# Optimization experiments

Measured on AMD Instinct MI355X. Metric: run time of the kernel, lower is better.

The kernel has to match this reference:

```python
import math
import jax, jax.numpy as jnp
import numpy as np

B, N = 1, 512
C_S, C_Z, H, C, P_Q, P_V = 384, 128, 12, 16, 4, 8
CAT = C_Z * H + C * H + 3 * H * P_V + 1  # 2017


def _apply(t_r, t_t, x):
    # t_r: (b,n,3,3), t_t: (b,n,3), x: (b,3,h,p,n) -> global frame coords
    xg = jnp.einsum('bnij,bjhpn->bihpn', t_r, x)
    return xg + jnp.swapaxes(t_t, 1, 2)[:, :, None, None, :]


def setup_inputs() -> dict:
    key = jax.random.key(0)
    ks = jax.random.split(key, 14)
    f = lambda k, shp: jax.random.normal(k, shp, dtype=jnp.float32)
    return {
        's': f(ks[0], (B, C_S, N)),
        'z': f(ks[1], (B, C_Z, N, N)),
        't_r': f(ks[2], (B, N, 3, 3)),
        't_t': f(ks[3], (B, N, 3)),
        'Wq': f(ks[4], (C * H, C_S)) * 0.02,
        'Wk': f(ks[5], (C * H, C_S)) * 0.02,
        'Wv': f(ks[6], (C * H, C_S)) * 0.02,
        'Wqp': f(ks[7], (3 * H * P_Q, C_S)) * 0.02,
        'Wkp': f(ks[8], (3 * H * P_Q, C_S)) * 0.02,
        'Wvp': f(ks[9], (3 * H * P_V, C_S)) * 0.02,
        'Wb': f(ks[10], (H, C_Z)) * 0.02,
        'gamma': f(ks[11], (H, 1, 1)) * 0.5,
        'Ws': f(ks[12], (C_S, CAT)) * 0.02,
        'bs': jnp.zeros((C_S,), dtype=jnp.float32),
    }


def reference(s, z, t_r, t_t, Wq, Wk, Wv, Wqp, Wkp, Wvp, Wb, gamma, Ws, bs):
    b, _, n = s.shape
    w_c = math.sqrt(2.0 / (9.0 * P_Q))
    w_l = math.sqrt(1.0 / 3.0)

    proj = lambda W: jnp.einsum('oc,bcn->bon', W, s)
    # torch rearrange 'b (c h) i -> b c h i' == reshape(b, c, h, n)
    q = proj(Wq).reshape(b, C, H, n)
    k = proj(Wk).reshape(b, C, H, n)
    v = proj(Wv).reshape(b, C, H, n)
    qp = proj(Wqp).reshape(b, 3, H, P_Q, n)
    kp = proj(Wkp).reshape(b, 3, H, P_Q, n)
    vp = proj(Wvp).reshape(b, 3, H, P_V, n)

    qg = _apply(t_r, t_t, qp)  # (b,3,h,p,n)
    kg = _apply(t_r, t_t, kp)
    diff = qg[..., :, None] - kg[..., None, :]          # (b,3,h,p,n,n)
    dist2 = jnp.sum(diff * diff, axis=(1, 3))           # sum coords + points -> (b,h,n,n)
    tmp = jax.nn.softplus(gamma)[None] * (w_c / 2.0) * dist2

    b_bias = jnp.einsum('hc,bcij->bhij', Wb, z)
    qk = jnp.einsum('bchi,bchj->bhij', q, k) / math.sqrt(C)
    a = jax.nn.softmax(w_l * (qk + b_bias - tmp), axis=-1)  # (b,h,n,n)

    o1 = jnp.einsum('bhij,bcij->bchi', a, z).reshape(b, C_Z * H, n)
    o2 = jnp.einsum('bhij,bchj->bchi', a, v).reshape(b, C * H, n)

    vg = _apply(t_r, t_t, vp)                           # (b,3,h,pv,n)
    o3g = jnp.einsum('bhij,bchpj->bchpi', a, vg)        # (b,3,h,pv,n)
    t_r_inv = jnp.swapaxes(t_r, -1, -2)
    t_t_inv = jnp.einsum('bnij,bnj->bni', -t_r_inv, t_t)
    o3 = _apply(t_r_inv, t_t_inv, o3g).reshape(b, 3 * H * P_V, n)
    o3_norm = jnp.linalg.norm(o3, axis=1, keepdims=True)  # (b,1,n)

    cat = jnp.concatenate([o1, o2, o3, o3_norm], axis=1)  # (b, CAT, n)
    return jnp.einsum('oc,bcn->bon', Ws, cat) + bs[None, :, None]
```

## Files before the change

kernel.cpp:

```cpp
#include <hip/hip_runtime.h>
#include <math.h>

#define N 512
#define H 12
#define CC 16
#define CZ 128
#define CS 384
#define PQ 4
#define PV 8
#define CATR 2017

__global__ __launch_bounds__(256) void k_proj(
    const float* __restrict__ s,
    const float* __restrict__ Wq, const float* __restrict__ Wk, const float* __restrict__ Wv,
    const float* __restrict__ Wqp, const float* __restrict__ Wkp, const float* __restrict__ Wvp,
    float* __restrict__ proj)
{
    __shared__ float Wt[16][33];
    __shared__ float St[32][128];
    int t = threadIdx.x;
    int o0 = blockIdx.x * 16;
    int n0 = blockIdx.y * 128;
    const float* Wsrc; int orow;
    if (o0 < 192)      { Wsrc = Wq;  orow = o0; }
    else if (o0 < 384) { Wsrc = Wk;  orow = o0-192; }
    else if (o0 < 576) { Wsrc = Wv;  orow = o0-384; }
    else if (o0 < 720) { Wsrc = Wqp; orow = o0-576; }
    else if (o0 < 864) { Wsrc = Wkp; orow = o0-720; }
    else               { Wsrc = Wvp; orow = o0-864; }

    int og = t >> 6, nl = t & 63;
    float acc[4][2] = {};
    for (int c0 = 0; c0 < CS; c0 += 32) {
        __syncthreads();
        for (int k = 0; k < 2; k++) {
            int idx = t + k*256;
            int oo = idx >> 5, ccol = idx & 31;
            Wt[oo][ccol] = Wsrc[(orow+oo)*CS + c0 + ccol];
        }
        for (int k = 0; k < 4; k++) {
            int idx = t + k*256;
            int ccr = idx >> 5, nn4 = idx & 31;
            float4 v = *(const float4*)&s[(c0+ccr)*N + n0 + nn4*4];
            *(float4*)&St[ccr][nn4*4] = v;
        }
        __syncthreads();
        for (int kk = 0; kk < 32; kk++) {
            float sv0 = St[kk][nl], sv1 = St[kk][nl+64];
            #pragma unroll
            for (int r = 0; r < 4; r++) {
                float w = Wt[og*4+r][kk];
                acc[r][0] += w * sv0;
                acc[r][1] += w * sv1;
            }
        }
    }
    float scale = (o0 < 192) ? 0.25f : 1.0f;
    for (int r = 0; r < 4; r++) {
        int o = o0 + og*4 + r;
        proj[o*N + n0 + nl]      = scale * acc[r][0];
        proj[o*N + n0 + 64 + nl] = scale * acc[r][1];
    }
}

__global__ void k_frames(const float* __restrict__ proj,
                         const float* __restrict__ t_r, const float* __restrict__ t_t,
                         float* __restrict__ qg, float* __restrict__ kg, float* __restrict__ vg)
{
    int gid = blockIdx.x * blockDim.x + threadIdx.x;
    int n = gid & (N-1);
    int hp = gid >> 9;
    if (hp >= 192) return;
    const float* src; float* dst; int rowb, stride;
    if (hp < 48)      { src = proj + 576*N; dst = qg; rowb = hp;    stride = 48; }
    else if (hp < 96) { src = proj + 720*N; dst = kg; rowb = hp-48; stride = 48; }
    else              { src = proj + 864*N; dst = vg; rowb = hp-96; stride = 96; }
    float x0 = src[(rowb + 0*stride)*N + n];
    float x1 = src[(rowb + 1*stride)*N + n];
    float x2 = src[(rowb + 2*stride)*N + n];
    #pragma unroll
    for (int d = 0; d < 3; d++) {
        float r0 = t_r[(n*3+d)*3+0], r1 = t_r[(n*3+d)*3+1], r2 = t_r[(n*3+d)*3+2];
        dst[(rowb + d*stride)*N + n] = r0*x0 + r1*x1 + r2*x2 + t_t[n*3+d];
    }
}

__global__ __launch_bounds__(512) void k_logits(
    const float* __restrict__ z, const float* __restrict__ proj,
    const float* __restrict__ qg, const float* __restrict__ kg,
    const float* __restrict__ Wb, const float* __restrict__ gamma,
    float* __restrict__ a)
{
    __shared__ float zt[16*512];
    __shared__ float pm[12][8];
    __shared__ float ps[12][8];
    const int i = blockIdx.x;
    const int t = threadIdx.x;
    const int w = t >> 6;
    const int l = t & 63;
    const size_t NN = (size_t)N * N;
    const float w_l  = 0.57735026918962584f;
    const float w_c2 = 0.11785113019775793f;

    float ch[12];
    #pragma unroll
    for (int h = 0; h < 12; ++h) {
        float g = gamma[h];
        float sp = (g > 20.f) ? g : log1pf(expf(g));
        ch[h] = sp * w_c2;
    }

    float acc[12] = {};

    {
        const float* qq = proj;
        const float* kk = proj + 192*N;
        for (int c = 0; c < 16; ++c) {
            float kv[12];
            #pragma unroll
            for (int h = 0; h < 12; ++h)
                kv[h] = kk[(size_t)(c*12+h)*N + t];
            #pragma unroll
            for (int h = 0; h < 12; ++h)
                acc[h] = fmaf(qq[(size_t)(c*12+h)*N + i], kv[h], acc[h]);
        }
    }
    {
        float k2[12] = {}, q2[12] = {};
        for (int dp = 0; dp < 12; ++dp) {
            int d = dp >> 2, p = dp & 3;
            #pragma unroll
            for (int h = 0; h < 12; ++h) {
                int r = (d*12 + h)*4 + p;
                float kv = kg[(size_t)r*N + t];
                float qv = qg[(size_t)r*N + i];
                acc[h] = fmaf(2.f*ch[h]*qv, kv, acc[h]);
                k2[h]  = fmaf(kv, kv, k2[h]);
                q2[h]  = fmaf(qv, qv, q2[h]);
            }
        }
        #pragma unroll
        for (int h = 0; h < 12; ++h)
            acc[h] = fmaf(-ch[h], k2[h] + q2[h], acc[h]);
    }

    {
        const int zc = t >> 5;
        const int zj = (t & 31) * 4;
        const float* zsrc = z + (size_t)zc*NN + (size_t)i*N + zj;
        float4 g0 = *(const float4*)(zsrc);
        float4 g1 = *(const float4*)(zsrc + 128);
        float4 g2 = *(const float4*)(zsrc + 256);
        float4 g3 = *(const float4*)(zsrc + 384);
        *(float4*)&zt[zc*512 + zj]       = g0;
        *(float4*)&zt[zc*512 + zj + 128] = g1;
        *(float4*)&zt[zc*512 + zj + 256] = g2;
        *(float4*)&zt[zc*512 + zj + 384] = g3;
        __syncthreads();
        for (int tb = 0; tb < 8; ++tb) {
            if (tb < 7) {
                const float* zn = zsrc + (size_t)(tb+1)*16*NN;
                g0 = *(const float4*)(zn);
                g1 = *(const float4*)(zn + 128);
                g2 = *(const float4*)(zn + 256);
                g3 = *(const float4*)(zn + 384);
            }
            #pragma unroll
            for (int c = 0; c < 16; ++c) {
                float zv = zt[c*512 + t];
                #pragma unroll
                for (int h = 0; h < 12; ++h)
                    acc[h] = fmaf(Wb[h*CZ + tb*16 + c], zv, acc[h]);
            }
            __syncthreads();
            if (tb < 7) {
                *(float4*)&zt[zc*512 + zj]       = g0;
                *(float4*)&zt[zc*512 + zj + 128] = g1;
                *(float4*)&zt[zc*512 + zj + 256] = g2;
                *(float4*)&zt[zc*512 + zj + 384] = g3;
                __syncthreads();
            }
        }
    }

    float lv[12], mw[12];
    #pragma unroll
    for (int h = 0; h < 12; ++h)
        lv[h] = w_l * acc[h];

    #pragma unroll
    for (int h = 0; h < 12; ++h) {
        float m = lv[h];
        for (int s = 32; s; s >>= 1) m = fmaxf(m, __shfl_xor(m, s));
        float e = __expf(lv[h] - m);
        float sm = e;
        for (int s = 32; s; s >>= 1) sm += __shfl_xor(sm, s);
        lv[h] = e; mw[h] = m;
        if (l == 0) { pm[h][w] = m; ps[h][w] = sm; }
    }
    __syncthreads();
    #pragma unroll
    for (int h = 0; h < 12; ++h) {
        float mg = pm[h][0];
        #pragma unroll
        for (int u = 1; u < 8; ++u) mg = fmaxf(mg, pm[h][u]);
        float sg = 0.f;
        #pragma unroll
        for (int u = 0; u < 8; ++u) sg += ps[h][u] * __expf(pm[h][u] - mg);
        float f = __expf(mw[h] - mg) / sg;
        a[((size_t)h*N + i)*N + t] = lv[h] * f;
    }
}

__global__ __launch_bounds__(256, 8) void k_o1(
    const float* __restrict__ a, const float* __restrict__ z,
    float* __restrict__ o1T)
{
    __shared__ float zls[64*36];
    __shared__ float als[12][36];
    const int i  = blockIdx.x;
    const int c0 = blockIdx.y * 64;
    const int t  = threadIdx.x;
    const int cg = t & 31, hg = (t >> 5) & 1, jq = t >> 6;

    float acc[2][6] = {};
    for (int jc = 0; jc < 16; ++jc) {
        __syncthreads();
        #pragma unroll
        for (int k = 0; k < 2; ++k) {
            int idx = t + k*256;
            int c = idx >> 3, j4 = idx & 7;
            *(float4*)&zls[c*36 + j4*4] =
                *(const float4*)&z[((size_t)(c0+c)*N + i)*N + jc*32 + j4*4];
        }
        if (t < 96) {
            int h = t >> 3, j4 = t & 7;
            *(float4*)&als[h][j4*4] =
                *(const float4*)&a[((size_t)h*N + i)*N + jc*32 + j4*4];
        }
        __syncthreads();
        #pragma unroll
        for (int s = 0; s < 2; ++s) {
            int jo = jq*8 + s*4;
            float4 a4[6];
            #pragma unroll
            for (int hh = 0; hh < 6; ++hh)
                a4[hh] = *(const float4*)&als[hg*6+hh][jo];
            #pragma unroll
            for (int r = 0; r < 2; ++r) {
                float4 z4 = *(const float4*)&zls[(cg + 32*r)*36 + jo];
                #pragma unroll
                for (int hh = 0; hh < 6; ++hh)
                    acc[r][hh] += z4.x*a4[hh].x + z4.y*a4[hh].y
                                + z4.z*a4[hh].z + z4.w*a4[hh].w;
            }
        }
    }
    const int sl = t & 63;
    __syncthreads();
    if (jq >= 2) {
        float* rb = &zls[(jq-2)*832 + sl*13];
        #pragma unroll
        for (int r = 0; r < 2; ++r)
            #pragma unroll
            for (int hh = 0; hh < 6; ++hh) rb[r*6+hh] = acc[r][hh];
    }
    __syncthreads();
    if (jq < 2) {
        const float* rb = &zls[jq*832 + sl*13];
        #pragma unroll
        for (int r = 0; r < 2; ++r)
            #pragma unroll
            for (int hh = 0; hh < 6; ++hh) acc[r][hh] += rb[r*6+hh];
    }
    __syncthreads();
    if (jq == 1) {
        float* rb = &zls[sl*13];
        #pragma unroll
        for (int r = 0; r < 2; ++r)
            #pragma unroll
            for (int hh = 0; hh < 6; ++hh) rb[r*6+hh] = acc[r][hh];
    }
    __syncthreads();
    if (jq == 0) {
        const float* rb = &zls[sl*13];
        #pragma unroll
        for (int r = 0; r < 2; ++r)
            #pragma unroll
            for (int hh = 0; hh < 3; ++hh) {
                int c = c0 + cg + 32*r, h = hg*6 + hh*2;
                float2 v2;
                v2.x = acc[r][hh*2]   + rb[r*6+hh*2];
                v2.y = acc[r][hh*2+1] + rb[r*6+hh*2+1];
                *(float2*)&o1T[(size_t)i*1536 + c*12 + h] = v2;
            }
    }
}

__global__ __launch_bounds__(256) void k_o2o3g(
    const float* __restrict__ a, const float* __restrict__ proj, const float* __restrict__ vg,
    float* __restrict__ catB, float* __restrict__ o3g)
{
    __shared__ float ats[8*132];
    __shared__ float vts[40*132];
    int h = blockIdx.x, i0 = blockIdx.y*8;
    int t = threadIdx.x;
    int il = t & 7, rg = (t>>3)&7, jq = t>>6;
    const float* v = proj + 384*N;
    float acc[5] = {};
    for (int jc = 0; jc < 4; jc++) {
        __syncthreads();
        {
            int ii = t >> 5, j4 = t & 31;
            *(float4*)&ats[ii*132 + j4*4] =
                *(const float4*)&a[((size_t)h*N + i0+ii)*N + jc*128 + j4*4];
        }
        #pragma unroll
        for (int k = 0; k < 5; k++) {
            int idx = t + k*256;
            int r = idx >> 5, j4 = idx & 31;
            const float* src = (r < 16) ? (v + (size_t)(r*H + h)*N)
                : (vg + (size_t)(((r-16)>>3)*96 + h*PV + ((r-16)&7))*N);
            *(float4*)&vts[r*132 + j4*4] = *(const float4*)&src[jc*128 + j4*4];
        }
        __syncthreads();
        #pragma unroll
        for (int s = 0; s < 8; s++) {
            int jo = jq*32 + s*4;
            float4 a4 = *(const float4*)&ats[il*132 + jo];
            #pragma unroll
            for (int r = 0; r < 5; r++) {
                float4 v4 = *(const float4*)&vts[(rg*5+r)*132 + jo];
                acc[r] += v4.x*a4.x + v4.y*a4.y + v4.z*a4.z + v4.w*a4.w;
            }
        }
    }
    __syncthreads();
    if (jq >= 2) {
        float* rb = &ats[((jq-2)*64 + (t & 63))*5];
        #pragma unroll
        for (int r = 0; r < 5; r++) rb[r] = acc[r];
    }
    __syncthreads();
    if (jq < 2) {
        const float* rb = &ats[(jq*64 + (t & 63))*5];
        #pragma unroll
        for (int r = 0; r < 5; r++) acc[r] += rb[r];
        if (jq == 1) {
            float* rb2 = &ats[640 + (t & 63)*5];
            #pragma unroll
            for (int r = 0; r < 5; r++) rb2[r] = acc[r];
        }
    }
    __syncthreads();
    if (jq == 0) {
        const float* rb2 = &ats[640 + t*5];
        #pragma unroll
        for (int r = 0; r < 5; r++) {
            float val = acc[r] + rb2[r];
            int row = rg*5 + r;
            if (row < 16) catB[(size_t)(row*H + h)*N + i0 + il] = val;
            else { int rr = row - 16;
                   o3g[(size_t)((rr>>3)*96 + h*PV + (rr&7))*N + i0 + il] = val; }
        }
    }
}

__global__ void k_o3(const float* __restrict__ o3g,
                     const float* __restrict__ t_r, const float* __restrict__ t_t,
                     float* __restrict__ catB)
{
    int gid = blockIdx.x*blockDim.x + threadIdx.x;
    int i = gid & (N-1), hp = gid >> 9;
    if (hp >= 96) return;
    float x0 = o3g[(size_t)(0*96 + hp)*N + i] - t_t[i*3+0];
    float x1 = o3g[(size_t)(1*96 + hp)*N + i] - t_t[i*3+1];
    float x2 = o3g[(size_t)(2*96 + hp)*N + i] - t_t[i*3+2];
    #pragma unroll
    for (int d = 0; d < 3; d++) {
        float o = t_r[(i*3+0)*3+d]*x0 + t_r[(i*3+1)*3+d]*x1 + t_r[(i*3+2)*3+d]*x2;
        catB[(size_t)(192 + d*96 + hp)*N + i] = o;
    }
}

__global__ void k_norm(float* __restrict__ catB)
{
    __shared__ float red[8][32];
    int il = threadIdx.x & 31, g = threadIdx.x >> 5;
    int i = blockIdx.x*32 + il;
    float acc = 0.f;
    for (int r = g*36; r < g*36 + 36; ++r) {
        float v = catB[(size_t)(192+r)*N + i];
        acc += v*v;
    }
    red[g][il] = acc;
    __syncthreads();
    if (g == 0) {
        acc = 0.f;
        #pragma unroll
        for (int u = 0; u < 8; ++u) acc += red[u][il];
        catB[(size_t)480*N + i] = sqrtf(acc);
    }
}

__global__ __launch_bounds__(256) void k_final(
    const float* __restrict__ Ws, const float* __restrict__ bs,
    const float* __restrict__ o1T, const float* __restrict__ catB,
    float* __restrict__ out)
{
    __shared__ float Wt[16*33];
    __shared__ float Ct[32*66];
    int o0 = blockIdx.x*16, n0 = blockIdx.y*64;
    int ks = blockIdx.z;
    int kbeg = ks*512, kend = min(CATR, kbeg+512);
    int t = threadIdx.x;
    int og = t >> 6, nl = t & 63;
    float acc[4] = {};
    for (int c0 = kbeg; c0 < kend; c0 += 32) {
        __syncthreads();
        for (int k = 0; k < 2; k++) {
            int idx = t + k*256;
            int oo = idx >> 5, ccol = idx & 31;
            int c = c0 + ccol;
            Wt[oo*33 + ccol] = (c < kend) ? Ws[(size_t)(o0+oo)*CATR + c] : 0.f;
        }
        if (ks < 3) {
            for (int k = 0; k < 2; k++) {
                int idx = t + k*256;
                int nn = idx >> 3, c4 = idx & 7;
                float4 v = *(const float4*)&o1T[(size_t)(n0+nn)*1536 + c0 + c4*4];
                Ct[(c4*4+0)*66 + nn] = v.x;
                Ct[(c4*4+1)*66 + nn] = v.y;
                Ct[(c4*4+2)*66 + nn] = v.z;
                Ct[(c4*4+3)*66 + nn] = v.w;
            }
        } else {
            for (int k = 0; k < 4; k++) {
                int idx = t + k*256;
                int ccr = idx >> 5, j2 = idx & 31;
                int c = c0 + ccr;
                float2 vv; vv.x = 0.f; vv.y = 0.f;
                if (c < kend) vv = *(const float2*)&catB[(size_t)(c-1536)*N + n0 + j2*2];
                *(float2*)&Ct[ccr*66 + j2*2] = vv;
            }
        }
        __syncthreads();
        int klim = min(32, kend - c0);
        for (int kk = 0; kk < klim; kk++) {
            float cv = Ct[kk*66 + nl];
            #pragma unroll
            for (int r = 0; r < 4; r++)
                acc[r] += Wt[(og*4+r)*33 + kk] * cv;
        }
    }
    #pragma unroll
    for (int r = 0; r < 4; r++) {
        int o = o0 + og*4 + r;
        float val = acc[r];
        if (ks == 0) val += bs[o];
        atomicAdd(&out[(size_t)o*N + n0 + nl], val);
    }
}

extern "C" void kernel_launch(void* const* d_in, const int* in_sizes, int n_in,
                              void* d_out, int out_size, void* d_ws, size_t ws_size,
                              hipStream_t stream)
{
    const float* s     = (const float*)d_in[0];
    const float* z     = (const float*)d_in[1];
    const float* t_r   = (const float*)d_in[2];
    const float* t_t   = (const float*)d_in[3];
    const float* Wq    = (const float*)d_in[4];
    const float* Wk    = (const float*)d_in[5];
    const float* Wv    = (const float*)d_in[6];
    const float* Wqp   = (const float*)d_in[7];
    const float* Wkp   = (const float*)d_in[8];
    const float* Wvp   = (const float*)d_in[9];
    const float* Wb    = (const float*)d_in[10];
    const float* gamma = (const float*)d_in[11];
    const float* Ws    = (const float*)d_in[12];
    const float* bs    = (const float*)d_in[13];
    float* out = (float*)d_out;

    float* ws   = (float*)d_ws;
    float* proj = ws;
    float* qg   = proj + 1152*N;
    float* kg   = qg   + 144*N;
    float* vg   = kg   + 144*N;
    float* o3g  = vg   + 288*N;
    float* a    = o3g  + 288*N;
    float* o1T  = a    + (size_t)H*N*N;
    float* catB = o1T  + (size_t)N*1536;

    k_proj   <<<dim3(72,4),   256, 0, stream>>>(s, Wq, Wk, Wv, Wqp, Wkp, Wvp, proj);
    k_frames <<<384,          256, 0, stream>>>(proj, t_r, t_t, qg, kg, vg);
    k_logits <<<512,          512, 0, stream>>>(z, proj, qg, kg, Wb, gamma, a);
    k_o1     <<<dim3(512,2),  256, 0, stream>>>(a, z, o1T);
    k_o2o3g  <<<dim3(12,64),  256, 0, stream>>>(a, proj, vg, catB, o3g);
    k_o3     <<<192,          256, 0, stream>>>(o3g, t_r, t_t, catB);
    k_norm   <<<16,           256, 0, stream>>>(catB);
    hipMemsetAsync(out, 0, (size_t)CS*N*sizeof(float), stream);
    k_final  <<<dim3(24,8,4), 256, 0, stream>>>(Ws, bs, o1T, catB, out);
}
```

Before: 390.0 us.

## Split QK and point-distance logits into a tiled augmented-GEMM kernel

```diff
diff --git a/kernel.cpp b/kernel.cpp
--- a/kernel.cpp
+++ b/kernel.cpp
@@ -85,10 +85,86 @@
     }
 }
 
-__global__ __launch_bounds__(512) void k_logits(
-    const float* __restrict__ z, const float* __restrict__ proj,
-    const float* __restrict__ qg, const float* __restrict__ kg,
-    const float* __restrict__ Wb, const float* __restrict__ gamma,
+__global__ __launch_bounds__(256) void k_qkgeom(
+    const float* __restrict__ proj, const float* __restrict__ qg,
+    const float* __restrict__ kg, const float* __restrict__ gamma,
+    float* __restrict__ a)
+{
+    __shared__ float Qe[30][32];
+    __shared__ float Ke[30][128];
+    const int h  = blockIdx.x;
+    const int i0 = blockIdx.y * 32;
+    const int j0 = blockIdx.z * 128;
+    const int t  = threadIdx.x;
+    const float w_c2 = 0.11785113019775793f;
+    float g = gamma[h];
+    float sp = (g > 20.f) ? g : log1pf(expf(g));
+    float ch = sp * w_c2;
+
+    for (int idx = t; idx < 28*32; idx += 256) {
+        int row = idx >> 5, col = idx & 31;
+        float v;
+        if (row < 16) v = proj[(size_t)(row*12 + h)*N + i0 + col];
+        else { int dp = row-16, d = dp>>2, p = dp&3;
+               v = 2.f*ch * qg[(size_t)(d*48 + h*4 + p)*N + i0 + col]; }
+        Qe[row][col] = v;
+    }
+    for (int idx = t; idx < 28*128; idx += 256) {
+        int row = idx >> 7, col = idx & 127;
+        float v;
+        if (row < 16) v = proj[(size_t)((192 + row*12 + h))*N + j0 + col];
+        else { int dp = row-16, d = dp>>2, p = dp&3;
+               v = kg[(size_t)(d*48 + h*4 + p)*N + j0 + col]; }
+        Ke[row][col] = v;
+    }
+    if (t < 32) {
+        float q2 = 0.f;
+        #pragma unroll
+        for (int dp = 0; dp < 12; ++dp) {
+            int d = dp>>2, p = dp&3;
+            float v = qg[(size_t)(d*48 + h*4 + p)*N + i0 + t];
+            q2 = fmaf(v, v, q2);
+        }
+        Qe[28][t] = 1.f;
+        Qe[29][t] = -ch * q2;
+    } else if (t < 160) {
+        int col = t - 32;
+        float k2 = 0.f;
+        #pragma unroll
+        for (int dp = 0; dp < 12; ++dp) {
+            int d = dp>>2, p = dp&3;
+            float v = kg[(size_t)(d*48 + h*4 + p)*N + j0 + col];
+            k2 = fmaf(v, v, k2);
+        }
+        Ke[28][col] = -ch * k2;
+        Ke[29][col] = 1.f;
+    }
+    __syncthreads();
+
+    const int tj = t & 31, ti = t >> 5;
+    float acc[4][4] = {};
+    #pragma unroll
+    for (int c = 0; c < 30; ++c) {
+        float4 k4 = *(const float4*)&Ke[c][tj*4];
+        float4 q4 = *(const float4*)&Qe[c][ti*4];
+        float qr[4] = {q4.x, q4.y, q4.z, q4.w};
+        #pragma unroll
+        for (int r = 0; r < 4; ++r) {
+            acc[r][0] = fmaf(qr[r], k4.x, acc[r][0]);
+            acc[r][1] = fmaf(qr[r], k4.y, acc[r][1]);
+            acc[r][2] = fmaf(qr[r], k4.z, acc[r][2]);
+            acc[r][3] = fmaf(qr[r], k4.w, acc[r][3]);
+        }
+    }
+    #pragma unroll
+    for (int r = 0; r < 4; ++r) {
+        float4 v; v.x = acc[r][0]; v.y = acc[r][1]; v.z = acc[r][2]; v.w = acc[r][3];
+        *(float4*)&a[((size_t)h*N + i0 + ti*4 + r)*N + j0 + tj*4] = v;
+    }
+}
+
+__global__ __launch_bounds__(512) void k_logits2(
+    const float* __restrict__ z, const float* __restrict__ Wb,
     float* __restrict__ a)
 {
     __shared__ float zt[16*512];
@@ -99,50 +175,12 @@
     const int w = t >> 6;
     const int l = t & 63;
     const size_t NN = (size_t)N * N;
-    const float w_l  = 0.57735026918962584f;
-    const float w_c2 = 0.11785113019775793f;
-
-    float ch[12];
-    #pragma unroll
-    for (int h = 0; h < 12; ++h) {
-        float g = gamma[h];
-        float sp = (g > 20.f) ? g : log1pf(expf(g));
-        ch[h] = sp * w_c2;
-    }
-
-    float acc[12] = {};
-
-    {
-        const float* qq = proj;
-        const float* kk = proj + 192*N;
-        for (int c = 0; c < 16; ++c) {
-            float kv[12];
-            #pragma unroll
-            for (int h = 0; h < 12; ++h)
-                kv[h] = kk[(size_t)(c*12+h)*N + t];
-            #pragma unroll
-            for (int h = 0; h < 12; ++h)
-                acc[h] = fmaf(qq[(size_t)(c*12+h)*N + i], kv[h], acc[h]);
-        }
-    }
-    {
-        float k2[12] = {}, q2[12] = {};
-        for (int dp = 0; dp < 12; ++dp) {
-            int d = dp >> 2, p = dp & 3;
-            #pragma unroll
-            for (int h = 0; h < 12; ++h) {
-                int r = (d*12 + h)*4 + p;
-                float kv = kg[(size_t)r*N + t];
-                float qv = qg[(size_t)r*N + i];
-                acc[h] = fmaf(2.f*ch[h]*qv, kv, acc[h]);
-                k2[h]  = fmaf(kv, kv, k2[h]);
-                q2[h]  = fmaf(qv, qv, q2[h]);
-            }
-        }
-        #pragma unroll
-        for (int h = 0; h < 12; ++h)
-            acc[h] = fmaf(-ch[h], k2[h] + q2[h], acc[h]);
-    }
+    const float w_l = 0.57735026918962584f;
+
+    float acc[12];
+    #pragma unroll
+    for (int h = 0; h < 12; ++h)
+        acc[h] = a[((size_t)h*N + i)*N + t];
 
     {
         const int zc = t >> 5;
@@ -492,13 +530,14 @@
     float* o1T  = a    + (size_t)H*N*N;
     float* catB = o1T  + (size_t)N*1536;
 
-    k_proj   <<<dim3(72,4),   256, 0, stream>>>(s, Wq, Wk, Wv, Wqp, Wkp, Wvp, proj);
-    k_frames <<<384,          256, 0, stream>>>(proj, t_r, t_t, qg, kg, vg);
-    k_logits <<<512,          512, 0, stream>>>(z, proj, qg, kg, Wb, gamma, a);
-    k_o1     <<<dim3(512,2),  256, 0, stream>>>(a, z, o1T);
-    k_o2o3g  <<<dim3(12,64),  256, 0, stream>>>(a, proj, vg, catB, o3g);
-    k_o3     <<<192,          256, 0, stream>>>(o3g, t_r, t_t, catB);
-    k_norm   <<<16,           256, 0, stream>>>(catB);
+    k_proj   <<<dim3(72,4),    256, 0, stream>>>(s, Wq, Wk, Wv, Wqp, Wkp, Wvp, proj);
+    k_frames <<<384,           256, 0, stream>>>(proj, t_r, t_t, qg, kg, vg);
+    k_qkgeom <<<dim3(12,16,4), 256, 0, stream>>>(proj, qg, kg, gamma, a);
+    k_logits2<<<512,           512, 0, stream>>>(z, Wb, a);
+    k_o1     <<<dim3(512,2),   256, 0, stream>>>(a, z, o1T);
+    k_o2o3g  <<<dim3(12,64),   256, 0, stream>>>(a, proj, vg, catB, o3g);
+    k_o3     <<<192,           256, 0, stream>>>(o3g, t_r, t_t, catB);
+    k_norm   <<<16,            256, 0, stream>>>(catB);
     hipMemsetAsync(out, 0, (size_t)CS*N*sizeof(float), stream);
-    k_final  <<<dim3(24,8,4), 256, 0, stream>>>(Ws, bs, o1T, catB, out);
-}
+    k_final  <<<dim3(24,8,4),  256, 0, stream>>>(Ws, bs, o1T, catB, out);
+}
```

New measurement: 375.9 us. 3.6% less time.
